# Kernel tuning notes

Measured on AMD Instinct MI355X. Metric: run time of the kernel, lower is better.

The kernel has to match this reference:

```python
import jax, jax.numpy as jnp
import numpy as np

DIM = 192
HEADS = 6
WS = (2, 7, 7)
SHIFT = (1, 3, 3)
MLP_HID = int(DIM * 4.0)
N = WS[0] * WS[1] * WS[2]  # 98


def _relative_position_index():
    wt, wh, ww = WS
    coords = np.stack(np.meshgrid(np.arange(wt), np.arange(wh), np.arange(ww), indexing='ij'))
    cf = coords.reshape(3, -1)  # (3, N)
    rel = cf[:, :, None] - cf[:, None, :]  # (3, N, N)
    rel = rel.transpose(1, 2, 0).copy()
    rel[:, :, 0] += wt - 1
    rel[:, :, 1] += wh - 1
    rel[:, :, 2] += ww - 1
    rel[:, :, 0] *= (2 * wh - 1) * (2 * ww - 1)
    rel[:, :, 1] *= 2 * ww - 1
    return rel.sum(-1)  # (N, N) int

RPI = jnp.asarray(_relative_position_index())


def setup_inputs() -> dict:
    key = jax.random.key(0)
    ks = jax.random.split(key, 12)
    B, C, T, H, W = 2, DIM, 8, 56, 56
    n_bias = (2 * WS[0] - 1) * (2 * WS[1] - 1) * (2 * WS[2] - 1)
    s = lambda k, shp, sd=0.02: jax.random.normal(k, shp, jnp.float32) * sd
    return {
        'x': jax.random.normal(ks[0], (B, C, T, H, W), jnp.float32),
        'mask_matrix': jnp.zeros((256, N, N), jnp.float32),
        'norm1_g': jnp.ones((DIM,), jnp.float32),
        'norm1_b': jnp.zeros((DIM,), jnp.float32),
        'qkv_w': s(ks[1], (DIM, 3 * DIM)),
        'qkv_b': jnp.zeros((3 * DIM,), jnp.float32),
        'proj_w': s(ks[2], (DIM, DIM)),
        'proj_b': jnp.zeros((DIM,), jnp.float32),
        'rpb_table': s(ks[3], (n_bias, HEADS)),
        'norm2_g': jnp.ones((DIM,), jnp.float32),
        'norm2_b': jnp.zeros((DIM,), jnp.float32),
        'fc1_w': s(ks[4], (DIM, MLP_HID)),
        'fc1_b': jnp.zeros((MLP_HID,), jnp.float32),
        'fc2_w': s(ks[5], (MLP_HID, DIM)),
        'fc2_b': jnp.zeros((DIM,), jnp.float32),
    }


def _layernorm(x, g, b, eps=1e-5):
    mu = jnp.mean(x, -1, keepdims=True)
    var = jnp.var(x, -1, keepdims=True)
    return (x - mu) * jax.lax.rsqrt(var + eps) * g + b


def _window_partition(x):
    # x: (B, T, H, W, C) -> (B*nW, N, C)
    B, T, H, W, C = x.shape
    wt, wh, ww = WS
    x = x.reshape(B, T // wt, wt, H // wh, wh, W // ww, ww, C)
    x = x.transpose(0, 1, 3, 5, 2, 4, 6, 7)
    return x.reshape(-1, wt * wh * ww, C)


def _window_reverse(win, B, T, H, W):
    wt, wh, ww = WS
    C = win.shape[-1]
    x = win.reshape(B, T // wt, H // wh, W // ww, wt, wh, ww, C)
    x = x.transpose(0, 1, 4, 2, 5, 3, 6, 7)
    return x.reshape(B, T, H, W, C)


def reference(x, mask_matrix, norm1_g, norm1_b, qkv_w, qkv_b, proj_w, proj_b,
              rpb_table, norm2_g, norm2_b, fc1_w, fc1_b, fc2_w, fc2_b):
    B, C, T, H, W = x.shape
    hd = C // HEADS
    scale = hd ** -0.5

    shortcut = x.transpose(0, 2, 3, 4, 1)  # (B,T,H,W,C) channel-last residual
    xn = _layernorm(shortcut, norm1_g, norm1_b)
    # cyclic shift
    xs = jnp.roll(xn, shift=(-SHIFT[0], -SHIFT[1], -SHIFT[2]), axis=(1, 2, 3))
    xw = _window_partition(xs)  # (B_, N, C)
    B_ = xw.shape[0]

    qkv = (xw @ qkv_w + qkv_b).reshape(B_, N, 3, HEADS, hd)
    q, k, v = (qkv[:, :, 0].transpose(0, 2, 1, 3),
               qkv[:, :, 1].transpose(0, 2, 1, 3),
               qkv[:, :, 2].transpose(0, 2, 1, 3))  # (B_, h, N, d)
    attn = jnp.einsum('bhnd,bhmd->bhnm', q * scale, k)
    bias = rpb_table[RPI.reshape(-1)].reshape(N, N, HEADS).transpose(2, 0, 1)
    attn = attn + bias[None]
    nW = mask_matrix.shape[0]
    attn = attn.reshape(B_ // nW, nW, HEADS, N, N) + mask_matrix[None, :, None]
    attn = jax.nn.softmax(attn.reshape(B_, HEADS, N, N), axis=-1)
    out = jnp.einsum('bhnm,bhmd->bhnd', attn, v).transpose(0, 2, 1, 3).reshape(B_, N, C)
    out = out @ proj_w + proj_b

    xr = _window_reverse(out, B, T, H, W)
    xr = jnp.roll(xr, shift=SHIFT, axis=(1, 2, 3))
    x1 = shortcut + xr

    xn2 = _layernorm(x1, norm2_g, norm2_b)
    h1 = jax.nn.gelu(xn2 @ fc1_w + fc1_b, approximate=False)
    x2 = x1 + (h1 @ fc2_w + fc2_b)
    return x2.transpose(0, 4, 1, 2, 3)  # (B, C, T, H, W)
```

## Files before the change

kernel.cpp:

```cpp
#include <hip/hip_runtime.h>
#include <hip/hip_bf16.h>
#include <math.h>

#define DEV __device__ __forceinline__

typedef __bf16 bf16;
typedef __bf16 bf16x8 __attribute__((ext_vector_type(8)));
typedef float f32x4 __attribute__((ext_vector_type(4)));

DEV f32x4 zero4() { f32x4 z; z[0]=0.f; z[1]=0.f; z[2]=0.f; z[3]=0.f; return z; }

DEV void gload_lds16(const bf16* g, bf16* l) {
    __builtin_amdgcn_global_load_lds(
        (const __attribute__((address_space(1))) void*)g,
        (__attribute__((address_space(3))) void*)l, 16, 0, 0);
}


__global__ __launch_bounds__(256) void prep_w_k(
    const float* __restrict__ qw, const float* __restrict__ pw,
    const float* __restrict__ f1, const float* __restrict__ f2,
    bf16* __restrict__ qwt, bf16* __restrict__ pwt,
    bf16* __restrict__ f1t, bf16* __restrict__ f2t)
{
    int i = blockIdx.x * 256 + threadIdx.x;
    if (i < 576*192) { int n = i / 192, k = i % 192; qwt[i] = (bf16)qw[(size_t)k*576 + n]; }
    if (i < 192*192) { int n = i / 192, k = i % 192; pwt[i] = (bf16)pw[(size_t)k*192 + n]; }
    if (i < 768*192) { int n = i / 192, k = i % 192; f1t[i] = (bf16)f1[(size_t)k*768 + n]; }
    if (i < 192*768) { int n = i / 768, k = i % 768; f2t[i] = (bf16)f2[(size_t)k*192 + n]; }
}

__global__ __launch_bounds__(256) void prep_bias_k(
    const float* __restrict__ rpb, float* __restrict__ biasT)
{
    int i = blockIdx.x * 256 + threadIdx.x;
    if (i >= 6*98*112) return;
    int nk = i % 112; int t = i / 112; int nq = t % 98; int h = t / 98;
    float v;
    if (nk < 98) {
        int t1 = nq/49, r1 = nq%49, h1 = r1/7, w1 = r1%7;
        int t2 = nk/49, r2 = nk%49, h2 = r2/7, w2 = r2%7;
        int idx = (t1 - t2 + 1)*169 + (h1 - h2 + 6)*13 + (w1 - w2 + 6);
        v = rpb[idx*6 + h];
    } else {
        v = -1e30f;
    }
    biasT[i] = v;
}

__global__ __launch_bounds__(256) void ln1_window_k(
    const float* __restrict__ x, const float* __restrict__ g,
    const float* __restrict__ bta, bf16* __restrict__ xw)
{
    __shared__ float tile[56*193];
    __shared__ float mu[56], rs[56];
    int blk = blockIdx.x;
    int bb = blk / 448; int r = blk % 448; int ts = r / 56; int hs = r % 56;
    int t = (ts + 1) & 7;
    int h = hs + 3; if (h >= 56) h -= 56;
    int tid = threadIdx.x;
    const float* xs = x + ((size_t)bb*1536 + t)*3136 + h*56;
    for (int e = tid; e < 192*56; e += 256) {
        int c = e / 56, w = e % 56;
        int wsp = w - 3; if (wsp < 0) wsp += 56;
        tile[wsp*193 + c] = xs[(size_t)c*25088 + w];
    }
    __syncthreads();
    if (tid < 224) {
        int row = tid >> 2, q = tid & 3;
        float s = 0.f, s2 = 0.f;
        for (int c = q*48; c < q*48 + 48; c++) {
            float v = tile[row*193 + c]; s += v; s2 += v*v;
        }
        s  += __shfl_xor(s, 1);  s  += __shfl_xor(s, 2);
        s2 += __shfl_xor(s2, 1); s2 += __shfl_xor(s2, 2);
        if (q == 0) {
            float m = s * (1.0f/192.0f);
            mu[row] = m;
            rs[row] = rsqrtf(s2 * (1.0f/192.0f) - m*m + 1e-5f);
        }
    }
    __syncthreads();
    int tb = ts >> 1, wt = ts & 1;
    int hb = hs / 7, wh = hs % 7;
    for (int e = tid; e < 56*192; e += 256) {
        int wpos = e / 192, c = e % 192;
        float v = (tile[wpos*193 + c] - mu[wpos]) * rs[wpos] * g[c] + bta[c];
        int wb = wpos / 7, ww = wpos % 7;
        int widx = bb*256 + tb*64 + hb*8 + wb;
        int n = wt*49 + wh*7 + ww;
        xw[((size_t)widx*98 + n)*192 + c] = (bf16)v;
    }
}

template<int KT, int NT, int EPI>
__global__ __launch_bounds__(256) void gemm_k(
    const bf16* __restrict__ A, const bf16* __restrict__ BT,
    const float* __restrict__ bias, const float* __restrict__ resid,
    void* __restrict__ outp)
{
    __shared__ bf16 la[2][128*64];
    __shared__ bf16 lb[2][64*64];
    constexpr int NTILES = NT / 64;
    constexpr int NK = KT / 64;
    constexpr int SPX = 392 / 8;
    int blk = blockIdx.x;
    int xcd = blk & 7, ix = blk >> 3;
    int m0 = (xcd * SPX + ix / NTILES) * 128;
    int n0 = (ix % NTILES) * 64;
    int tid = threadIdx.x;
    int lane = tid & 63;
    int wv = tid >> 6;
    int wr = wv >> 1, wc = wv & 1;
    int l15 = lane & 15, lg = lane >> 4;

    auto stage = [&](int kt, int buf) {
        int kb = kt * 64;
        #pragma unroll
        for (int t = 0; t < 4; t++) {
            int e = t*256 + wv*64 + lane;
            int row = e >> 3, ck = e & 7;
            gload_lds16(&A[(size_t)(m0 + row)*KT + kb + ((ck ^ (row & 7)) << 3)],
                        &la[buf][(t*256 + wv*64) * 8]);
        }
        #pragma unroll
        for (int t = 0; t < 2; t++) {
            int e = t*256 + wv*64 + lane;
            int row = e >> 3, ck = e & 7;
            gload_lds16(&BT[(size_t)(n0 + row)*KT + kb + ((ck ^ (row & 7)) << 3)],
                        &lb[buf][(t*256 + wv*64) * 8]);
        }
    };

    f32x4 acc[4][2];
    #pragma unroll
    for (int i = 0; i < 4; i++)
        #pragma unroll
        for (int j = 0; j < 2; j++) acc[i][j] = zero4();

    stage(0, 0);
    __syncthreads();

    for (int kt = 0; kt < NK; kt++) {
        int cur = kt & 1;
        if (kt + 1 < NK) stage(kt + 1, cur ^ 1);
        const bf16* lab = la[cur];
        const bf16* lbb = lb[cur];
        #pragma unroll
        for (int ks = 0; ks < 64; ks += 32) {
            int lc = (ks >> 3) + lg;
            bf16x8 af[4], bfr[2];
            #pragma unroll
            for (int i = 0; i < 4; i++) {
                int ri = wr*64 + i*16 + l15;
                af[i] = *(const bf16x8*)&lab[ri*64 + ((lc ^ (ri & 7)) << 3)];
            }
            #pragma unroll
            for (int j = 0; j < 2; j++) {
                int rj = wc*32 + j*16 + l15;
                bfr[j] = *(const bf16x8*)&lbb[rj*64 + ((lc ^ (rj & 7)) << 3)];
            }
            #pragma unroll
            for (int i = 0; i < 4; i++)
                #pragma unroll
                for (int j = 0; j < 2; j++)
                    acc[i][j] = __builtin_amdgcn_mfma_f32_16x16x32_bf16(af[i], bfr[j], acc[i][j], 0, 0, 0);
        }
        __syncthreads();
    }

    if constexpr (EPI == 4) {
        #pragma unroll
        for (int i = 0; i < 4; i++) {
            #pragma unroll
            for (int j = 0; j < 2; j++) {
                int row0 = m0 + wr*64 + i*16 + lg*4;
                int col = n0 + wc*32 + j*16 + l15;
                f32x4 o;
                #pragma unroll
                for (int r = 0; r < 4; r++)
                    o[r] = acc[i][j][r] + bias[col] + resid[(size_t)(row0 + r)*NT + col];
                int bb2 = row0 >= 25088;
                size_t off = (size_t)bb2*192*25088 + (size_t)col*25088 + (row0 - bb2*25088);
                *(f32x4*)&((float*)outp)[off] = o;
            }
        }
    } else {
        #pragma unroll
        for (int i = 0; i < 4; i++) {
            #pragma unroll
            for (int j = 0; j < 2; j++) {
                #pragma unroll
                for (int r = 0; r < 4; r++) {
                    int row = m0 + wr*64 + i*16 + lg*4 + r;
                    int col = n0 + wc*32 + j*16 + l15;
                    float v = acc[i][j][r] + bias[col];
                    size_t oidx = (size_t)row * NT + col;
                    if constexpr (EPI == 0) {
                        ((bf16*)outp)[oidx] = (bf16)v;
                    } else if constexpr (EPI == 1) {
                        ((float*)outp)[oidx] = v;
                    } else if constexpr (EPI == 2) {
                        float gl = 0.5f * v * (1.0f + erff(v * 0.70710678118654752f));
                        ((bf16*)outp)[oidx] = (bf16)gl;
                    }
                }
            }
        }
    }
}

__global__ __launch_bounds__(128) void attn_k(
    const bf16* __restrict__ qkv, const float* __restrict__ biasT,
    const float* __restrict__ maskm, bf16* __restrict__ aout)
{
    __shared__ bf16 VT[32*128];
    __shared__ bf16 Pl[2*16*136];
    int blk = blockIdx.x;
    int t8 = (blk & 7) * 384 + (blk >> 3);
    int b_ = t8 / 6, head = t8 % 6;
    int tid = threadIdx.x, lane = tid & 63, wv = tid >> 6;
    int l15 = lane & 15, lg = (lane >> 4) & 3;
    int wib = b_ & 255;
    const bf16* base = qkv + (size_t)b_*98*576;

    {
        unsigned int* vz = (unsigned int*)VT;
        for (int e = tid; e < 2048; e += 128) vz[e] = 0u;
        unsigned int* pz = (unsigned int*)Pl;
        for (int e = tid; e < 256; e += 128) {
            int w2 = e >> 7, rem = e & 127;
            int row = rem >> 3, cp = rem & 7;
            pz[(w2*16 + row)*68 + 56 + cp] = 0u;
        }
    }
    __syncthreads();
    {
        int dq = tid >> 5;
        int kl = tid & 31;
        const bf16* vbase = base + 384 + head*32 + dq*8;
        #pragma unroll
        for (int kr = 0; kr < 4; kr++) {
            int k = kr*32 + kl;
            if (k < 98) {
                bf16x8 v8 = *(const bf16x8*)&vbase[(size_t)k*576];
                #pragma unroll
                for (int j = 0; j < 8; j++)
                    VT[(dq*8 + j)*128 + (k ^ (j << 3))] = v8[j];
            }
        }
    }
    __syncthreads();

    bf16x8 kfr[7];
    #pragma unroll
    for (int j = 0; j < 7; j++) {
        int krow = j*16 + l15; if (krow > 97) krow = 97;
        kfr[j] = *(const bf16x8*)&base[(size_t)krow*576 + 192 + head*32 + lg*8];
    }

    const float scale = 0.17677669529663687f;
    bf16* Pw = Pl + wv*16*136;
    const int rt0 = wv ? 4 : 0, rt1 = wv ? 7 : 4;

    auto loadQ = [&](int rt) {
        int qrow = rt*16 + l15; if (qrow > 97) qrow = 97;
        return *(const bf16x8*)&base[(size_t)qrow*576 + head*32 + lg*8];
    };
    bf16x8 qf = loadQ(rt0);

    #pragma unroll 1
    for (int rt = rt0; rt < rt1; rt++) {
        bf16x8 qnext = qf;
        if (rt + 1 < rt1) qnext = loadQ(rt + 1);
        f32x4 sacc[7];
        #pragma unroll
        for (int j = 0; j < 7; j++) sacc[j] = zero4();
        #pragma unroll
        for (int j = 0; j < 7; j++)
            sacc[j] = __builtin_amdgcn_mfma_f32_16x16x32_bf16(qf, kfr[j], sacc[j], 0, 0, 0);
        #pragma unroll
        for (int r = 0; r < 4; r++) {
            int nq = rt*16 + lg*4 + r;
            int nqc = nq > 97 ? 97 : nq;
            const float* bb = biasT + (head*98 + nqc)*112;
            const float* mm = maskm + ((size_t)wib*98 + nqc)*98;
            float sv[7];
            float m = -1e30f;
            #pragma unroll
            for (int j = 0; j < 7; j++) {
                int nk = j*16 + l15;
                float v = sacc[j][r]*scale + bb[nk];
                if (nk < 98) v += mm[nk];
                sv[j] = v; m = fmaxf(m, v);
            }
            #pragma unroll
            for (int d = 1; d < 16; d <<= 1) m = fmaxf(m, __shfl_xor(m, d));
            float sum = 0.f;
            #pragma unroll
            for (int j = 0; j < 7; j++) { sv[j] = __expf(sv[j] - m); sum += sv[j]; }
            #pragma unroll
            for (int d = 1; d < 16; d <<= 1) sum += __shfl_xor(sum, d);
            float inv = 1.0f / sum;
            #pragma unroll
            for (int j = 0; j < 7; j++)
                Pw[(lg*4 + r)*136 + j*16 + l15] = (bf16)(sv[j]*inv);
        }
        #pragma unroll
        for (int dt = 0; dt < 2; dt++) {
            int dl = dt*16 + l15;
            int xr = (dl & 7) << 3;
            f32x4 oacc = zero4();
            #pragma unroll
            for (int kc = 0; kc < 4; kc++) {
                bf16x8 pf = *(const bf16x8*)&Pw[l15*136 + kc*32 + lg*8];
                bf16x8 vf = *(const bf16x8*)&VT[dl*128 + ((kc*32 + lg*8) ^ xr)];
                oacc = __builtin_amdgcn_mfma_f32_16x16x32_bf16(pf, vf, oacc, 0, 0, 0);
            }
            #pragma unroll
            for (int r = 0; r < 4; r++) {
                int row = rt*16 + lg*4 + r;
                if (row < 98)
                    aout[((size_t)b_*98 + row)*192 + head*32 + dt*16 + l15] = (bf16)oacc[r];
            }
        }
        qf = qnext;
    }
}

__global__ __launch_bounds__(256) void rev_res_ln2_k(
    const float* __restrict__ x, const float* __restrict__ pw,
    const float* __restrict__ g2, const float* __restrict__ b2,
    float* __restrict__ x1, bf16* __restrict__ xn2)
{
    __shared__ float tile[56*193];
    __shared__ float mu[56], rs[56];
    int blk = blockIdx.x;
    int bb = blk / 448; int r = blk % 448; int t = r / 56; int h = r % 56;
    int ts = (t + 7) & 7;
    int hs = h - 3; if (hs < 0) hs += 56;
    int tid = threadIdx.x;
    const float* xs = x + ((size_t)bb*1536 + t)*3136 + h*56;
    for (int e = tid; e < 192*56; e += 256) {
        int c = e / 56, w = e % 56;
        tile[w*193 + c] = xs[(size_t)c*25088 + w];
    }
    __syncthreads();
    int tb = ts >> 1, wt = ts & 1, hb = hs / 7, wh = hs % 7;
    for (int e = tid; e < 56*192; e += 256) {
        int w = e / 192, c = e % 192;
        int wsp = w - 3; if (wsp < 0) wsp += 56;
        int wb = wsp / 7, ww = wsp % 7;
        size_t tok = (size_t)(bb*256 + tb*64 + hb*8 + wb)*98 + wt*49 + wh*7 + ww;
        tile[w*193 + c] += pw[tok*192 + c];
    }
    __syncthreads();
    if (tid < 224) {
        int row = tid >> 2, q = tid & 3;
        float s = 0.f, s2 = 0.f;
        for (int c = q*48; c < q*48 + 48; c++) {
            float v = tile[row*193 + c]; s += v; s2 += v*v;
        }
        s  += __shfl_xor(s, 1);  s  += __shfl_xor(s, 2);
        s2 += __shfl_xor(s2, 1); s2 += __shfl_xor(s2, 2);
        if (q == 0) {
            float m = s * (1.0f/192.0f);
            mu[row] = m;
            rs[row] = rsqrtf(s2 * (1.0f/192.0f) - m*m + 1e-5f);
        }
    }
    __syncthreads();
    size_t tok0 = ((size_t)(bb*8 + t)*56 + h)*56;
    for (int e = tid; e < 56*192; e += 256) {
        int w = e / 192, c = e % 192;
        float v = tile[w*193 + c];
        x1[(tok0 + w)*192 + c] = v;
        xn2[(tok0 + w)*192 + c] = (bf16)((v - mu[w]) * rs[w] * g2[c] + b2[c]);
    }
}

extern "C" void kernel_launch(void* const* d_in, const int* in_sizes, int n_in,
                              void* d_out, int out_size, void* d_ws, size_t ws_size,
                              hipStream_t stream)
{
    const float* x     = (const float*)d_in[0];
    const float* maskm = (const float*)d_in[1];
    const float* n1g   = (const float*)d_in[2];
    const float* n1b   = (const float*)d_in[3];
    const float* qkvw  = (const float*)d_in[4];
    const float* qkvb  = (const float*)d_in[5];
    const float* projw = (const float*)d_in[6];
    const float* projb = (const float*)d_in[7];
    const float* rpb   = (const float*)d_in[8];
    const float* n2g   = (const float*)d_in[9];
    const float* n2b   = (const float*)d_in[10];
    const float* f1w   = (const float*)d_in[11];
    const float* f1b   = (const float*)d_in[12];
    const float* f2w   = (const float*)d_in[13];
    const float* f2b   = (const float*)d_in[14];

    char* ws = (char*)d_ws;
    bf16*  qkv_wt  = (bf16*)(ws + 0);
    bf16*  proj_wt = (bf16*)(ws + 221184);
    bf16*  fc1_wt  = (bf16*)(ws + 294912);
    bf16*  fc2_wt  = (bf16*)(ws + 589824);
    float* biasT   = (float*)(ws + 884736);
    bf16* xw   = (bf16*)(ws + 1179648);
    bf16* aout = xw;
    char* Bp = ws + 1179648 + 19267584;
    bf16*  qkv  = (bf16*)Bp;
    float* pwin = (float*)Bp;
    char* Cp = Bp + 57802752;
    float* x1  = (float*)Cp;
    bf16*  xn2 = (bf16*)(Cp + 38535168);
    bf16*  h1  = (bf16*)(Cp + 38535168 + 19267584);

    prep_w_k<<<576, 256, 0, stream>>>(qkvw, projw, f1w, f2w, qkv_wt, proj_wt, fc1_wt, fc2_wt);
    prep_bias_k<<<258, 256, 0, stream>>>(rpb, biasT);
    ln1_window_k<<<896, 256, 0, stream>>>(x, n1g, n1b, xw);
    gemm_k<192, 576, 0><<<392*9, 256, 0, stream>>>(xw, qkv_wt, qkvb, nullptr, qkv);
    attn_k<<<3072, 128, 0, stream>>>(qkv, biasT, maskm, aout);
    gemm_k<192, 192, 1><<<392*3, 256, 0, stream>>>(aout, proj_wt, projb, nullptr, pwin);
    rev_res_ln2_k<<<896, 256, 0, stream>>>(x, pwin, n2g, n2b, x1, xn2);
    gemm_k<192, 768, 2><<<392*12, 256, 0, stream>>>(xn2, fc1_wt, f1b, nullptr, h1);
    gemm_k<768, 192, 4><<<392*3, 256, 0, stream>>>(h1, fc2_wt, f2b, x1, (float*)d_out);
}
```

Baseline: 241.9 us.

## Pre-swizzle bias and mask into MFMA fragment layout for vector loads

Adds prep kernels that rearrange the relative-position bias and the attention mask into the per-lane MFMA accumulator layout. The attention kernel can then fetch them with contiguous 16-byte loads instead of scattered per-element gathers, and it runs the softmax on all four rows together as vectors. This costs an extra pass over the 256-window mask each call and a padded mask buffer (about 12.8 MB) placed in the h1 workspace region.

```diff
diff --git a/kernel.cpp b/kernel.cpp
--- a/kernel.cpp
+++ b/kernel.cpp
@@ -30,22 +30,47 @@
     if (i < 192*768) { int n = i / 768, k = i % 768; f2t[i] = (bf16)f2[(size_t)k*192 + n]; }
 }
 
-__global__ __launch_bounds__(256) void prep_bias_k(
-    const float* __restrict__ rpb, float* __restrict__ biasT)
+__global__ __launch_bounds__(256) void prep_biasF_k(
+    const float* __restrict__ rpb, float* __restrict__ biasF)
 {
     int i = blockIdx.x * 256 + threadIdx.x;
-    if (i >= 6*98*112) return;
-    int nk = i % 112; int t = i / 112; int nq = t % 98; int h = t / 98;
-    float v;
-    if (nk < 98) {
-        int t1 = nq/49, r1 = nq%49, h1 = r1/7, w1 = r1%7;
-        int t2 = nk/49, r2 = nk%49, h2 = r2/7, w2 = r2%7;
-        int idx = (t1 - t2 + 1)*169 + (h1 - h2 + 6)*13 + (w1 - w2 + 6);
-        v = rpb[idx*6 + h];
-    } else {
-        v = -1e30f;
-    }
-    biasT[i] = v;
+    if (i >= 6*7*7*64) return;
+    int lane = i & 63; int g = i >> 6;
+    int j = g % 7; g /= 7; int rt = g % 7; int head = g / 7;
+    int l15 = lane & 15, lg = lane >> 4;
+    int nk = j*16 + l15;
+    f32x4 o;
+    #pragma unroll
+    for (int r = 0; r < 4; r++) {
+        int nq = rt*16 + lg*4 + r; if (nq > 97) nq = 97;
+        if (nk < 98) {
+            int t1 = nq/49, r1 = nq%49, h1 = r1/7, w1 = r1%7;
+            int t2 = nk/49, r2 = nk%49, h2 = r2/7, w2 = r2%7;
+            int idx = (t1 - t2 + 1)*169 + (h1 - h2 + 6)*13 + (w1 - w2 + 6);
+            o[r] = rpb[idx*6 + head];
+        } else {
+            o[r] = -1e30f;
+        }
+    }
+    *(f32x4*)&biasF[(size_t)i*4] = o;
+}
+
+__global__ __launch_bounds__(256) void prep_maskF_k(
+    const float* __restrict__ maskm, float* __restrict__ maskF)
+{
+    int i = blockIdx.x * 256 + threadIdx.x;
+    if (i >= 256*7*7*64) return;
+    int lane = i & 63; int g = i >> 6;
+    int j = g % 7; g /= 7; int rt = g % 7; int wib = g / 7;
+    int l15 = lane & 15, lg = lane >> 4;
+    int nk = j*16 + l15;
+    f32x4 o;
+    #pragma unroll
+    for (int r = 0; r < 4; r++) {
+        int nq = rt*16 + lg*4 + r; if (nq > 97) nq = 97;
+        o[r] = (nk < 98) ? maskm[((size_t)wib*98 + nq)*98 + nk] : 0.f;
+    }
+    *(f32x4*)&maskF[(size_t)i*4] = o;
 }
 
 __global__ __launch_bounds__(256) void ln1_window_k(
@@ -211,8 +236,8 @@
 }
 
 __global__ __launch_bounds__(128) void attn_k(
-    const bf16* __restrict__ qkv, const float* __restrict__ biasT,
-    const float* __restrict__ maskm, bf16* __restrict__ aout)
+    const bf16* __restrict__ qkv, const float* __restrict__ biasF,
+    const float* __restrict__ maskF, bf16* __restrict__ aout)
 {
     __shared__ bf16 VT[32*128];
     __shared__ bf16 Pl[2*16*136];
@@ -279,32 +304,46 @@
         #pragma unroll
         for (int j = 0; j < 7; j++)
             sacc[j] = __builtin_amdgcn_mfma_f32_16x16x32_bf16(qf, kfr[j], sacc[j], 0, 0, 0);
-        #pragma unroll
-        for (int r = 0; r < 4; r++) {
-            int nq = rt*16 + lg*4 + r;
-            int nqc = nq > 97 ? 97 : nq;
-            const float* bb = biasT + (head*98 + nqc)*112;
-            const float* mm = maskm + ((size_t)wib*98 + nqc)*98;
-            float sv[7];
-            float m = -1e30f;
+        {
+            const float* bfp = biasF + ((size_t)(head*7 + rt)*7)*256 + lane*4;
+            const float* mfp = maskF + ((size_t)(wib*7 + rt)*7)*256 + lane*4;
             #pragma unroll
             for (int j = 0; j < 7; j++) {
-                int nk = j*16 + l15;
-                float v = sacc[j][r]*scale + bb[nk];
-                if (nk < 98) v += mm[nk];
-                sv[j] = v; m = fmaxf(m, v);
-            }
-            #pragma unroll
-            for (int d = 1; d < 16; d <<= 1) m = fmaxf(m, __shfl_xor(m, d));
-            float sum = 0.f;
-            #pragma unroll
-            for (int j = 0; j < 7; j++) { sv[j] = __expf(sv[j] - m); sum += sv[j]; }
-            #pragma unroll
-            for (int d = 1; d < 16; d <<= 1) sum += __shfl_xor(sum, d);
-            float inv = 1.0f / sum;
+                f32x4 bv = *(const f32x4*)&bfp[j*256];
+                f32x4 mv = *(const f32x4*)&mfp[j*256];
+                sacc[j] = sacc[j]*scale + bv + mv;
+            }
+            f32x4 m4 = sacc[0];
+            #pragma unroll
+            for (int j = 1; j < 7; j++) {
+                #pragma unroll
+                for (int r = 0; r < 4; r++) m4[r] = fmaxf(m4[r], sacc[j][r]);
+            }
+            #pragma unroll
+            for (int d = 1; d < 16; d <<= 1) {
+                #pragma unroll
+                for (int r = 0; r < 4; r++) m4[r] = fmaxf(m4[r], __shfl_xor(m4[r], d));
+            }
+            f32x4 s4 = zero4();
+            #pragma unroll
+            for (int j = 0; j < 7; j++) {
+                #pragma unroll
+                for (int r = 0; r < 4; r++) sacc[j][r] = __expf(sacc[j][r] - m4[r]);
+                s4 += sacc[j];
+            }
+            #pragma unroll
+            for (int d = 1; d < 16; d <<= 1) {
+                #pragma unroll
+                for (int r = 0; r < 4; r++) s4[r] += __shfl_xor(s4[r], d);
+            }
+            f32x4 inv4;
+            #pragma unroll
+            for (int r = 0; r < 4; r++) inv4[r] = 1.0f / s4[r];
             #pragma unroll
             for (int j = 0; j < 7; j++)
-                Pw[(lg*4 + r)*136 + j*16 + l15] = (bf16)(sv[j]*inv);
+                #pragma unroll
+                for (int r = 0; r < 4; r++)
+                    Pw[(lg*4 + r)*136 + j*16 + l15] = (bf16)(sacc[j][r]*inv4[r]);
         }
         #pragma unroll
         for (int dt = 0; dt < 2; dt++) {
@@ -404,7 +443,7 @@
     bf16*  proj_wt = (bf16*)(ws + 221184);
     bf16*  fc1_wt  = (bf16*)(ws + 294912);
     bf16*  fc2_wt  = (bf16*)(ws + 589824);
-    float* biasT   = (float*)(ws + 884736);
+    float* biasF   = (float*)(ws + 884736);
     bf16* xw   = (bf16*)(ws + 1179648);
     bf16* aout = xw;
     char* Bp = ws + 1179648 + 19267584;
@@ -414,12 +453,14 @@
     float* x1  = (float*)Cp;
     bf16*  xn2 = (bf16*)(Cp + 38535168);
     bf16*  h1  = (bf16*)(Cp + 38535168 + 19267584);
+    float* maskF = (float*)(Cp + 38535168 + 19267584);
 
     prep_w_k<<<576, 256, 0, stream>>>(qkvw, projw, f1w, f2w, qkv_wt, proj_wt, fc1_wt, fc2_wt);
-    prep_bias_k<<<258, 256, 0, stream>>>(rpb, biasT);
+    prep_biasF_k<<<74, 256, 0, stream>>>(rpb, biasF);
+    prep_maskF_k<<<3136, 256, 0, stream>>>(maskm, maskF);
     ln1_window_k<<<896, 256, 0, stream>>>(x, n1g, n1b, xw);
     gemm_k<192, 576, 0><<<392*9, 256, 0, stream>>>(xw, qkv_wt, qkvb, nullptr, qkv);
-    attn_k<<<3072, 128, 0, stream>>>(qkv, biasT, maskm, aout);
+    attn_k<<<3072, 128, 0, stream>>>(qkv, biasF, maskF, aout);
     gemm_k<192, 192, 1><<<392*3, 256, 0, stream>>>(aout, proj_wt, projb, nullptr, pwin);
     rev_res_ln2_k<<<896, 256, 0, stream>>>(x, pwin, n2g, n2b, x1, xn2);
     gemm_k<192, 768, 2><<<392*12, 256, 0, stream>>>(xn2, fc1_wt, f1b, nullptr, h1);
```

New measurement: 236.2 us. 1.02x faster.
